# Performance work log

Measured on AMD Instinct MI355X. Metric: run time of the kernel, lower is better.

The kernel has to match this reference:

```python
import jax, jax.numpy as jnp
import numpy as np
import math

B, S, D, H = 2, 2048, 1024, 16
DH = D // H
MASK_VALUE = -1e6


def setup_inputs() -> dict:
    key = jax.random.key(0)
    ks = jax.random.split(key, 6)
    x = jax.random.normal(ks[0], (B, S, D), dtype=jnp.float32)
    scale = 1.0 / math.sqrt(D)
    Wq = jax.random.normal(ks[1], (D, D), dtype=jnp.float32) * scale
    Wk = jax.random.normal(ks[2], (D, D), dtype=jnp.float32) * scale
    Wv = jax.random.normal(ks[3], (D, D), dtype=jnp.float32) * scale
    Wo = jax.random.normal(ks[4], (D, D), dtype=jnp.float32) * scale
    valid_lens = jax.random.randint(ks[5], (B,), 1, S + 1, dtype=jnp.int32)
    return {"x": x, "Wq": Wq, "Wk": Wk, "Wv": Wv, "Wo": Wo, "valid_lens": valid_lens}


def reference(x, Wq, Wk, Wv, Wo, valid_lens):
    # Projections (Linear with bias=False): [B,S,D] -> split into H heads of DH
    def split_heads(y):
        return y.reshape(B, S, H, DH).transpose(0, 2, 1, 3)  # [B,H,S,DH]

    q = split_heads(x @ Wq)
    k = split_heads(x @ Wk)
    v = split_heads(x @ Wv)

    # scores [B,H,Sq,Sk]; masking depends only on key position per batch
    scores = jnp.einsum("bhqd,bhkd->bhqk", q, k) / math.sqrt(DH)
    key_pos = jnp.arange(S, dtype=jnp.int32)  # [Sk]
    mask = key_pos[None, None, None, :] < valid_lens[:, None, None, None]
    scores = jnp.where(mask, scores, MASK_VALUE)
    attn = jax.nn.softmax(scores, axis=-1)  # dropout is identity in eval

    out = jnp.einsum("bhqk,bhkd->bhqd", attn, v)  # [B,H,S,DH]
    out = out.transpose(0, 2, 1, 3).reshape(B, S, D)  # concat heads
    return out @ Wo
```

## Files before the change

### kernel.cpp

```cpp
#include <hip/hip_runtime.h>

#define Bdim 2
#define Sdim 2048
#define Ddim 1024
#define Hdim 16

typedef unsigned short u16;
typedef u16 u16x8 __attribute__((ext_vector_type(8)));
typedef u16 u16x4 __attribute__((ext_vector_type(4)));
typedef unsigned u32x4 __attribute__((ext_vector_type(4)));
typedef __bf16 bf16x8 __attribute__((ext_vector_type(8)));
typedef float f32x4 __attribute__((ext_vector_type(4)));
typedef float f32x16 __attribute__((ext_vector_type(16)));

static __device__ __forceinline__ u16 f2bf(float f) {
  unsigned u = __float_as_uint(f);
  u += 0x7fffu + ((u >> 16) & 1u);
  return (u16)(u >> 16);
}
static __device__ __forceinline__ float bf2f(u16 v) {
  return __uint_as_float((unsigned)v << 16);
}
static __device__ __forceinline__ bf16x8 asbf(u16x8 v) {
  return __builtin_bit_cast(bf16x8, v);
}
static __device__ __forceinline__ f32x4 mfma16(bf16x8 a, bf16x8 b, f32x4 c) {
  return __builtin_amdgcn_mfma_f32_16x16x32_bf16(a, b, c, 0, 0, 0);
}
static __device__ __forceinline__ f32x16 mfma32(bf16x8 a, bf16x8 b, f32x16 c) {
  return __builtin_amdgcn_mfma_f32_32x32x16_bf16(a, b, c, 0, 0, 0);
}

__global__ __launch_bounds__(256) void cvtx(const float* __restrict__ x,
                                            u16* __restrict__ xb) {
  int i = blockIdx.x * 256 + threadIdx.x;
  const float4* xp = (const float4*)x;
  float4 a = xp[2 * i], b = xp[2 * i + 1];
  u16x8 o;
  o[0] = f2bf(a.x); o[1] = f2bf(a.y); o[2] = f2bf(a.z); o[3] = f2bf(a.w);
  o[4] = f2bf(b.x); o[5] = f2bf(b.y); o[6] = f2bf(b.z); o[7] = f2bf(b.w);
  ((u16x8*)xb)[i] = o;
}

__global__ __launch_bounds__(256) void transw(
    const float* __restrict__ W0, const float* __restrict__ W1,
    const float* __restrict__ W2, const float* __restrict__ W3,
    u16* __restrict__ T0, u16* __restrict__ T1,
    u16* __restrict__ T2, u16* __restrict__ T3) {
  const float* W = blockIdx.z == 0 ? W0 : blockIdx.z == 1 ? W1 : blockIdx.z == 2 ? W2 : W3;
  u16* T = blockIdx.z == 0 ? T0 : blockIdx.z == 1 ? T1 : blockIdx.z == 2 ? T2 : T3;
  __shared__ float tile[32][33];
  const int t = threadIdx.x;
  const int k0 = blockIdx.x * 32, n0 = blockIdx.y * 32;
  const int r = t >> 3, cq = (t & 7) * 4;
  float4 v = *(const float4*)(W + (size_t)(k0 + r) * Ddim + n0 + cq);
  tile[r][cq] = v.x; tile[r][cq + 1] = v.y; tile[r][cq + 2] = v.z; tile[r][cq + 3] = v.w;
  __syncthreads();
  u16x4 ov;
  ov[0] = f2bf(tile[cq][r]);
  ov[1] = f2bf(tile[cq + 1][r]);
  ov[2] = f2bf(tile[cq + 2][r]);
  ov[3] = f2bf(tile[cq + 3][r]);
  *(u16x4*)(T + (size_t)(n0 + r) * Ddim + k0 + cq) = ov;
}

__global__ __launch_bounds__(256) void vtrans(const u16* __restrict__ V,
                                              u16* __restrict__ Vt) {
  __shared__ u16 tile[32][72];
  const int t = threadIdx.x;
  const int s0 = blockIdx.x * 32;
  const int bh = blockIdx.y, b = bh >> 4, h = bh & 15;
  {
    int sl = t >> 3, dq = (t & 7) * 8;
    u16x8 v = *(const u16x8*)(V + (size_t)(b * Sdim + s0 + sl) * Ddim + h * 64 + dq);
    *(u16x8*)(&tile[sl][dq]) = v;
  }
  __syncthreads();
  {
    int dl = t >> 2, sq = (t & 3) * 8;
    u16x8 v;
#pragma unroll
    for (int i = 0; i < 8; i++) v[i] = tile[sq + i][dl];
    int s = s0 + sq;
    int kt = s >> 6, c = (s >> 3) & 7;
    *(u16x8*)(Vt + ((((size_t)bh * 32 + kt) * 8 + c) * 64 + dl) * 8) = v;
  }
}

__global__ __launch_bounds__(256) void tilek(const u16* __restrict__ K,
                                             u16* __restrict__ Kt) {
  int tid = blockIdx.x * 256 + threadIdx.x;
  int row = tid & 63;
  int c = (tid >> 6) & 7;
  int kt = (tid >> 9) & 31;
  int bh = tid >> 14;
  int b = bh >> 4, h = bh & 15;
  u16x8 kc = *(const u16x8*)(K + (size_t)(b * Sdim + kt * 64 + row) * Ddim + h * 64 + c * 8);
  ((u16x8*)Kt)[tid] = kc;
}

template <bool F32OUT>
__global__ __launch_bounds__(256) void gemm128(
    const u16* __restrict__ A,
    const u16* __restrict__ Bt0, const u16* __restrict__ Bt1, const u16* __restrict__ Bt2,
    void* __restrict__ C0v, void* __restrict__ C1v, void* __restrict__ C2v) {
  __shared__ u16 As[128 * 64];
  __shared__ u16 Bs[128 * 64];
  const int zz = blockIdx.y >> 3;
  const u16* Bt = (zz == 0) ? Bt0 : (zz == 1) ? Bt1 : Bt2;
  void* Cv = (zz == 0) ? C0v : (zz == 1) ? C1v : C2v;

  const int t = threadIdx.x;
  const int lane = t & 63, w = t >> 6;
  const int wm = w >> 1, wn = w & 1;
  const int c = lane & 15, g = lane >> 4;
  const int m0 = blockIdx.x * 128, n0 = (blockIdx.y & 7) * 128;
  const float oscale = (!F32OUT && zz == 0) ? 0.125f : 1.0f;

  const f32x4 zv = {0.f, 0.f, 0.f, 0.f};
  f32x4 acc[4][4];
#pragma unroll
  for (int m = 0; m < 4; m++)
#pragma unroll
    for (int n = 0; n < 4; n++) acc[m][n] = zv;

  for (int kt = 0; kt < 1024; kt += 64) {
    __syncthreads();
#pragma unroll
    for (int i = 0; i < 4; i++) {
      int idx = t + 256 * i;
      int row = idx >> 3, ch = idx & 7;
      int sw = (ch ^ (row & 7)) * 8;
      u16x8 va = *(const u16x8*)(A + (size_t)(m0 + row) * 1024 + kt + ch * 8);
      *(u16x8*)(As + row * 64 + sw) = va;
      u16x8 vb = *(const u16x8*)(Bt + (size_t)(n0 + row) * 1024 + kt + ch * 8);
      *(u16x8*)(Bs + row * 64 + sw) = vb;
    }
    __syncthreads();
#pragma unroll
    for (int kh = 0; kh < 2; kh++) {
      bf16x8 af[4], bfr[4];
#pragma unroll
      for (int m = 0; m < 4; m++) {
        int row = wm * 64 + m * 16 + c;
        int chr = kh * 4 + g;
        af[m] = asbf(*(const u16x8*)(As + row * 64 + ((chr ^ (row & 7)) * 8)));
      }
#pragma unroll
      for (int n = 0; n < 4; n++) {
        int row = wn * 64 + n * 16 + c;
        int chr = kh * 4 + g;
        bfr[n] = asbf(*(const u16x8*)(Bs + row * 64 + ((chr ^ (row & 7)) * 8)));
      }
#pragma unroll
      for (int m = 0; m < 4; m++)
#pragma unroll
        for (int n = 0; n < 4; n++) acc[m][n] = mfma16(af[m], bfr[n], acc[m][n]);
    }
  }
#pragma unroll
  for (int m = 0; m < 4; m++)
#pragma unroll
    for (int n = 0; n < 4; n++)
#pragma unroll
      for (int r = 0; r < 4; r++) {
        int row = m0 + wm * 64 + m * 16 + 4 * g + r;
        int col = n0 + wn * 64 + n * 16 + c;
        if (F32OUT)
          ((float*)Cv)[(size_t)row * 1024 + col] = acc[m][n][r];
        else
          ((u16*)Cv)[(size_t)row * 1024 + col] = f2bf(acc[m][n][r] * oscale);
      }
}

__global__ __launch_bounds__(64, 4) void attn_kernel(
    const u16* __restrict__ Q, const u16* __restrict__ Kt,
    const u16* __restrict__ Vt, const int* __restrict__ vlen,
    u16* __restrict__ O, u16* __restrict__ Opart, float2* __restrict__ mlp) {
  __shared__ u16 ot[32][72];
  const int lane = threadIdx.x;
  const int q = lane & 31, hi = lane >> 5;
  const int bh = blockIdx.y, b = bh >> 4, h = bh & 15;
  const int q0 = blockIdx.x * 32;
  const int nv = vlen[b];
  const int NS = gridDim.z, z = blockIdx.z;

  bf16x8 qf[4];
  {
    const u16* qp = Q + (size_t)(b * Sdim + q0 + q) * Ddim + h * 64 + hi * 8;
#pragma unroll
    for (int s = 0; s < 4; s++) qf[s] = asbf(*(const u16x8*)(qp + s * 16));
  }

  f32x16 o0, o1;
#pragma unroll
  for (int r = 0; r < 16; r++) { o0[r] = 0.f; o1[r] = 0.f; }
  float m = -3.0e38f, l = 0.f;

  const int nt = (nv + 63) >> 6;
  const int chunk = (nt + NS - 1) / NS;
  const int t0 = z * chunk;
  const int t1 = min(nt, t0 + chunk);
  for (int kt = t0; kt < t1; ++kt) {
    const int k0 = kt * 64;
    const u16* Ktile = Kt + ((size_t)bh * 32 + kt) * 4096;
    const u16* Vtile = Vt + ((size_t)bh * 32 + kt) * 4096;
    f32x16 sc[2];
#pragma unroll
    for (int kb = 0; kb < 2; kb++) {
      f32x16 acc;
#pragma unroll
      for (int r = 0; r < 16; r++) acc[r] = 0.f;
#pragma unroll
      for (int s = 0; s < 4; s++) {
        bf16x8 kf = asbf(*(const u16x8*)(Ktile + (2 * s + hi) * 512 + (kb * 32 + q) * 8));
        acc = mfma32(kf, qf[s], acc);
      }
      sc[kb] = acc;
    }
    if (k0 + 64 > nv) {
#pragma unroll
      for (int kb = 0; kb < 2; kb++)
#pragma unroll
        for (int r = 0; r < 16; r++) {
          int key = k0 + kb * 32 + (r & 3) + 8 * (r >> 2) + 4 * hi;
          if (key >= nv) sc[kb][r] = -1e30f;
        }
    }
    float mx[16];
#pragma unroll
    for (int r = 0; r < 16; r++) mx[r] = fmaxf(sc[0][r], sc[1][r]);
#pragma unroll
    for (int st = 8; st > 0; st >>= 1)
#pragma unroll
      for (int r = 0; r < st; r++) mx[r] = fmaxf(mx[r], mx[r + st]);
    float tm = fmaxf(mx[0], __shfl_xor(mx[0], 32));
    if (!__all(tm <= m + 8.f)) {
      float mn = fmaxf(m, tm);
      float al = __expf(m - mn);
#pragma unroll
      for (int r = 0; r < 16; r++) { o0[r] *= al; o1[r] *= al; }
      l *= al;
      m = mn;
    }
    unsigned pw[4][4];
    float s0 = 0.f, s1 = 0.f, s2 = 0.f, s3 = 0.f;
#pragma unroll
    for (int kb = 0; kb < 2; kb++)
#pragma unroll
      for (int hh = 0; hh < 2; hh++)
#pragma unroll
        for (int wi = 0; wi < 4; wi++) {
          float e0 = __expf(sc[kb][hh * 8 + wi * 2] - m);
          float e1 = __expf(sc[kb][hh * 8 + wi * 2 + 1] - m);
          if (wi == 0) s0 += e0 + e1;
          else if (wi == 1) s1 += e0 + e1;
          else if (wi == 2) s2 += e0 + e1;
          else s3 += e0 + e1;
          asm("v_cvt_pk_bf16_f32 %0, %1, %2"
              : "=v"(pw[kb * 2 + hh][wi]) : "v"(e0), "v"(e1));
        }
    float ssum = (s0 + s1) + (s2 + s3);
    ssum += __shfl_xor(ssum, 32);
    l += ssum;
#pragma unroll
    for (int f = 0; f < 4; f++) {
      asm("v_permlane32_swap_b32 %0, %1" : "+v"(pw[f][0]), "+v"(pw[f][2]));
      asm("v_permlane32_swap_b32 %0, %1" : "+v"(pw[f][1]), "+v"(pw[f][3]));
    }
#pragma unroll
    for (int f = 0; f < 4; f++) {
      u32x4 wv = {pw[f][0], pw[f][1], pw[f][2], pw[f][3]};
      bf16x8 pa = __builtin_bit_cast(bf16x8, wv);
      bf16x8 va = asbf(*(const u16x8*)(Vtile + (2 * f + hi) * 512 + q * 8));
      bf16x8 vb = asbf(*(const u16x8*)(Vtile + (2 * f + hi) * 512 + (32 + q) * 8));
      o0 = mfma32(va, pa, o0);
      o1 = mfma32(vb, pa, o1);
    }
  }
  const float scale = (NS == 1) ? (1.f / l) : 1.f;
#pragma unroll
  for (int r = 0; r < 16; r++) {
    const int dh = (r & 3) + 8 * (r >> 2) + 4 * hi;
    ot[q][dh] = f2bf(o0[r] * scale);
    ot[q][32 + dh] = f2bf(o1[r] * scale);
  }
  asm volatile("s_waitcnt lgkmcnt(0)" ::: "memory");
  __builtin_amdgcn_sched_barrier(0);
  if (NS == 1) {
    u16* op = O + (size_t)(b * Sdim + q0 + q) * Ddim + h * 64 + hi * 32;
#pragma unroll
    for (int j = 0; j < 4; j++)
      *(u16x8*)(op + j * 8) = *(const u16x8*)(&ot[q][hi * 32 + j * 8]);
  } else {
    u16* op = Opart + ((size_t)(z * 32 + bh) * Sdim + q0 + q) * 64 + hi * 32;
#pragma unroll
    for (int j = 0; j < 4; j++)
      *(u16x8*)(op + j * 8) = *(const u16x8*)(&ot[q][hi * 32 + j * 8]);
    if (hi == 0)
      mlp[(size_t)(z * 32 + bh) * Sdim + q0 + q] = make_float2(m, l);
  }
}

template <int NS>
__global__ __launch_bounds__(256) void attn_combine(
    const u16* __restrict__ Opart, const float2* __restrict__ mlp,
    u16* __restrict__ O) {
  const int t = threadIdx.x;
  const int bh = blockIdx.y, b = bh >> 4, h = bh & 15;
  const int q = blockIdx.x * 32 + (t >> 3);
  const int d0 = (t & 7) * 8;
  float2 ml[NS];
  float M = -3.0e38f;
#pragma unroll
  for (int z = 0; z < NS; z++) {
    ml[z] = mlp[(size_t)(z * 32 + bh) * Sdim + q];
    M = fmaxf(M, ml[z].x);
  }
  float acc[8];
#pragma unroll
  for (int i = 0; i < 8; i++) acc[i] = 0.f;
  float wsum = 0.f;
#pragma unroll
  for (int z = 0; z < NS; z++) {
    float w = __expf(ml[z].x - M);
    wsum += w * ml[z].y;
    u16x8 ov = *(const u16x8*)(Opart + ((size_t)(z * 32 + bh) * Sdim + q) * 64 + d0);
#pragma unroll
    for (int i = 0; i < 8; i++) acc[i] += w * bf2f(ov[i]);
  }
  const float inv = 1.f / wsum;
  u16x8 res;
#pragma unroll
  for (int i = 0; i < 8; i++) res[i] = f2bf(acc[i] * inv);
  *(u16x8*)(O + ((size_t)b * Sdim + q) * Ddim + h * 64 + d0) = res;
}

extern "C" void kernel_launch(void* const* d_in, const int* in_sizes, int n_in,
                              void* d_out, int out_size, void* d_ws, size_t ws_size,
                              hipStream_t stream) {
  const float* x = (const float*)d_in[0];
  const float* Wq = (const float*)d_in[1];
  const float* Wk = (const float*)d_in[2];
  const float* Wv = (const float*)d_in[3];
  const float* Wo = (const float*)d_in[4];
  const int* vl = (const int*)d_in[5];
  float* out = (float*)d_out;

  char* ws = (char*)d_ws;
  const size_t SZ_X = (size_t)Bdim * Sdim * Ddim * sizeof(u16);
  const size_t SZ_W = (size_t)Ddim * Ddim * sizeof(u16);
  u16* xb = (u16*)ws; ws += SZ_X;
  u16* WqT = (u16*)ws; ws += SZ_W;
  u16* WkT = (u16*)ws; ws += SZ_W;
  u16* WvT = (u16*)ws; ws += SZ_W;
  u16* WoT = (u16*)ws; ws += SZ_W;
  u16* Qb = (u16*)ws; ws += SZ_X;
  u16* Kb = (u16*)ws; ws += SZ_X;
  u16* Vb = (u16*)ws; ws += SZ_X;
  u16* Ob = (u16*)ws; ws += SZ_X;
  u16* Ktb = (u16*)ws; ws += SZ_X;
  u16* Vtb = (u16*)ws; ws += SZ_X;

  const size_t PER_SPLIT = (size_t)Bdim * Hdim * Sdim * 64 * sizeof(u16) +
                           (size_t)Bdim * Hdim * Sdim * sizeof(float2);
  size_t used = (size_t)(ws - (char*)d_ws);
  size_t avail = (ws_size > used) ? ws_size - used : 0;
  int NS = (avail >= 4 * PER_SPLIT) ? 4 : (avail >= 2 * PER_SPLIT) ? 2 : 1;
  u16* Opart = (u16*)ws;
  float2* mlp = (float2*)(ws + (size_t)NS * Bdim * Hdim * Sdim * 64 * sizeof(u16));

  cvtx<<<dim3((Bdim * Sdim * Ddim) / (8 * 256)), 256, 0, stream>>>(x, xb);
  transw<<<dim3(32, 32, 4), 256, 0, stream>>>(Wq, Wk, Wv, Wo, WqT, WkT, WvT, WoT);
  gemm128<false><<<dim3(32, 24), 256, 0, stream>>>(xb, WqT, WkT, WvT, Qb, Kb, Vb);
  vtrans<<<dim3(Sdim / 32, Bdim * Hdim), 256, 0, stream>>>(Vb, Vtb);
  tilek<<<dim3((Bdim * Sdim * Ddim / 8) / 256), 256, 0, stream>>>(Kb, Ktb);
  attn_kernel<<<dim3(Sdim / 32, Bdim * Hdim, NS), 64, 0, stream>>>(Qb, Ktb, Vtb, vl, Ob,
                                                                   Opart, mlp);
  if (NS == 4)
    attn_combine<4><<<dim3(Sdim / 32, Bdim * Hdim), 256, 0, stream>>>(Opart, mlp, Ob);
  else if (NS == 2)
    attn_combine<2><<<dim3(Sdim / 32, Bdim * Hdim), 256, 0, stream>>>(Opart, mlp, Ob);
  gemm128<true><<<dim3(32, 8), 256, 0, stream>>>(Ob, WoT, WoT, WoT, out, out, out);
}
```

Baseline: 130.3 us.

## Store GEMM operands in MFMA-fragment order and load fragments directly from global

```diff
diff --git a/kernel.cpp b/kernel.cpp
--- a/kernel.cpp
+++ b/kernel.cpp
@@ -31,15 +31,22 @@
   return __builtin_amdgcn_mfma_f32_32x32x16_bf16(a, b, c, 0, 0, 0);
 }
 
+static __device__ __forceinline__ size_t ftcell(int R, int k) {
+  return ((((((size_t)(R >> 7) * 16 + (k >> 6)) * 2 + ((R >> 6) & 1)) * 4 +
+            ((R >> 4) & 3)) * 2 + ((k >> 5) & 1)) * 4 + ((k >> 3) & 3)) * 16 +
+         (R & 15);
+}
+
 __global__ __launch_bounds__(256) void cvtx(const float* __restrict__ x,
-                                            u16* __restrict__ xb) {
+                                            u16* __restrict__ xf) {
   int i = blockIdx.x * 256 + threadIdx.x;
   const float4* xp = (const float4*)x;
   float4 a = xp[2 * i], b = xp[2 * i + 1];
   u16x8 o;
   o[0] = f2bf(a.x); o[1] = f2bf(a.y); o[2] = f2bf(a.z); o[3] = f2bf(a.w);
   o[4] = f2bf(b.x); o[5] = f2bf(b.y); o[6] = f2bf(b.z); o[7] = f2bf(b.w);
-  ((u16x8*)xb)[i] = o;
+  int R = i >> 7, k = (i & 127) * 8;
+  ((u16x8*)xf)[ftcell(R, k)] = o;
 }
 
 __global__ __launch_bounds__(256) void transw(
@@ -61,7 +68,8 @@
   ov[1] = f2bf(tile[cq + 1][r]);
   ov[2] = f2bf(tile[cq + 2][r]);
   ov[3] = f2bf(tile[cq + 3][r]);
-  *(u16x4*)(T + (size_t)(n0 + r) * Ddim + k0 + cq) = ov;
+  int n = n0 + r, k = k0 + cq;
+  *(u16x4*)(T + ftcell(n, k) * 8 + (k & 7)) = ov;
 }
 
 __global__ __launch_bounds__(256) void vtrans(const u16* __restrict__ V,
@@ -100,12 +108,10 @@
 }
 
 template <bool F32OUT>
-__global__ __launch_bounds__(256) void gemm128(
+__global__ __launch_bounds__(256, 4) void gemm128(
     const u16* __restrict__ A,
     const u16* __restrict__ Bt0, const u16* __restrict__ Bt1, const u16* __restrict__ Bt2,
     void* __restrict__ C0v, void* __restrict__ C1v, void* __restrict__ C2v) {
-  __shared__ u16 As[128 * 64];
-  __shared__ u16 Bs[128 * 64];
   const int zz = blockIdx.y >> 3;
   const u16* Bt = (zz == 0) ? Bt0 : (zz == 1) ? Bt1 : Bt2;
   void* Cv = (zz == 0) ? C0v : (zz == 1) ? C1v : C2v;
@@ -114,7 +120,7 @@
   const int lane = t & 63, w = t >> 6;
   const int wm = w >> 1, wn = w & 1;
   const int c = lane & 15, g = lane >> 4;
-  const int m0 = blockIdx.x * 128, n0 = (blockIdx.y & 7) * 128;
+  const int mb = blockIdx.x, nb = blockIdx.y & 7;
   const float oscale = (!F32OUT && zz == 0) ? 0.125f : 1.0f;
 
   const f32x4 zv = {0.f, 0.f, 0.f, 0.f};
@@ -124,33 +130,21 @@
 #pragma unroll
     for (int n = 0; n < 4; n++) acc[m][n] = zv;
 
-  for (int kt = 0; kt < 1024; kt += 64) {
-    __syncthreads();
-#pragma unroll
-    for (int i = 0; i < 4; i++) {
-      int idx = t + 256 * i;
-      int row = idx >> 3, ch = idx & 7;
-      int sw = (ch ^ (row & 7)) * 8;
-      u16x8 va = *(const u16x8*)(A + (size_t)(m0 + row) * 1024 + kt + ch * 8);
-      *(u16x8*)(As + row * 64 + sw) = va;
-      u16x8 vb = *(const u16x8*)(Bt + (size_t)(n0 + row) * 1024 + kt + ch * 8);
-      *(u16x8*)(Bs + row * 64 + sw) = vb;
-    }
-    __syncthreads();
+  const u16* Abase = A + (size_t)lane * 8;
+  const u16* Bbase = Bt + (size_t)lane * 8;
+  for (int kt = 0; kt < 16; ++kt) {
 #pragma unroll
     for (int kh = 0; kh < 2; kh++) {
       bf16x8 af[4], bfr[4];
 #pragma unroll
       for (int m = 0; m < 4; m++) {
-        int row = wm * 64 + m * 16 + c;
-        int chr = kh * 4 + g;
-        af[m] = asbf(*(const u16x8*)(As + row * 64 + ((chr ^ (row & 7)) * 8)));
+        size_t X = ((((size_t)mb * 16 + kt) * 2 + wm) * 4 + m) * 2 + kh;
+        af[m] = asbf(*(const u16x8*)(Abase + X * 512));
       }
 #pragma unroll
       for (int n = 0; n < 4; n++) {
-        int row = wn * 64 + n * 16 + c;
-        int chr = kh * 4 + g;
-        bfr[n] = asbf(*(const u16x8*)(Bs + row * 64 + ((chr ^ (row & 7)) * 8)));
+        size_t Y = ((((size_t)nb * 16 + kt) * 2 + wn) * 4 + n) * 2 + kh;
+        bfr[n] = asbf(*(const u16x8*)(Bbase + Y * 512));
       }
 #pragma unroll
       for (int m = 0; m < 4; m++)
@@ -164,8 +158,8 @@
     for (int n = 0; n < 4; n++)
 #pragma unroll
       for (int r = 0; r < 4; r++) {
-        int row = m0 + wm * 64 + m * 16 + 4 * g + r;
-        int col = n0 + wn * 64 + n * 16 + c;
+        int row = mb * 128 + wm * 64 + m * 16 + 4 * g + r;
+        int col = nb * 128 + wn * 64 + n * 16 + c;
         if (F32OUT)
           ((float*)Cv)[(size_t)row * 1024 + col] = acc[m][n][r];
         else
@@ -288,10 +282,12 @@
   asm volatile("s_waitcnt lgkmcnt(0)" ::: "memory");
   __builtin_amdgcn_sched_barrier(0);
   if (NS == 1) {
-    u16* op = O + (size_t)(b * Sdim + q0 + q) * Ddim + h * 64 + hi * 32;
-#pragma unroll
-    for (int j = 0; j < 4; j++)
-      *(u16x8*)(op + j * 8) = *(const u16x8*)(&ot[q][hi * 32 + j * 8]);
+    int R = b * Sdim + q0 + q;
+#pragma unroll
+    for (int j = 0; j < 4; j++) {
+      int k = h * 64 + hi * 32 + j * 8;
+      ((u16x8*)O)[ftcell(R, k)] = *(const u16x8*)(&ot[q][hi * 32 + j * 8]);
+    }
   } else {
     u16* op = Opart + ((size_t)(z * 32 + bh) * Sdim + q0 + q) * 64 + hi * 32;
 #pragma unroll
@@ -333,7 +329,8 @@
   u16x8 res;
 #pragma unroll
   for (int i = 0; i < 8; i++) res[i] = f2bf(acc[i] * inv);
-  *(u16x8*)(O + ((size_t)b * Sdim + q) * Ddim + h * 64 + d0) = res;
+  int R = b * Sdim + q, k = h * 64 + d0;
+  ((u16x8*)O)[ftcell(R, k)] = res;
 }
 
 extern "C" void kernel_launch(void* const* d_in, const int* in_sizes, int n_in,
@@ -350,7 +347,7 @@
   char* ws = (char*)d_ws;
   const size_t SZ_X = (size_t)Bdim * Sdim * Ddim * sizeof(u16);
   const size_t SZ_W = (size_t)Ddim * Ddim * sizeof(u16);
-  u16* xb = (u16*)ws; ws += SZ_X;
+  u16* xf = (u16*)ws; ws += SZ_X;
   u16* WqT = (u16*)ws; ws += SZ_W;
   u16* WkT = (u16*)ws; ws += SZ_W;
   u16* WvT = (u16*)ws; ws += SZ_W;
@@ -358,7 +355,7 @@
   u16* Qb = (u16*)ws; ws += SZ_X;
   u16* Kb = (u16*)ws; ws += SZ_X;
   u16* Vb = (u16*)ws; ws += SZ_X;
-  u16* Ob = (u16*)ws; ws += SZ_X;
+  u16* Obf = (u16*)ws; ws += SZ_X;
   u16* Ktb = (u16*)ws; ws += SZ_X;
   u16* Vtb = (u16*)ws; ws += SZ_X;
 
@@ -370,16 +367,16 @@
   u16* Opart = (u16*)ws;
   float2* mlp = (float2*)(ws + (size_t)NS * Bdim * Hdim * Sdim * 64 * sizeof(u16));
 
-  cvtx<<<dim3((Bdim * Sdim * Ddim) / (8 * 256)), 256, 0, stream>>>(x, xb);
+  cvtx<<<dim3((Bdim * Sdim * Ddim) / (8 * 256)), 256, 0, stream>>>(x, xf);
   transw<<<dim3(32, 32, 4), 256, 0, stream>>>(Wq, Wk, Wv, Wo, WqT, WkT, WvT, WoT);
-  gemm128<false><<<dim3(32, 24), 256, 0, stream>>>(xb, WqT, WkT, WvT, Qb, Kb, Vb);
+  gemm128<false><<<dim3(32, 24), 256, 0, stream>>>(xf, WqT, WkT, WvT, Qb, Kb, Vb);
   vtrans<<<dim3(Sdim / 32, Bdim * Hdim), 256, 0, stream>>>(Vb, Vtb);
   tilek<<<dim3((Bdim * Sdim * Ddim / 8) / 256), 256, 0, stream>>>(Kb, Ktb);
-  attn_kernel<<<dim3(Sdim / 32, Bdim * Hdim, NS), 64, 0, stream>>>(Qb, Ktb, Vtb, vl, Ob,
+  attn_kernel<<<dim3(Sdim / 32, Bdim * Hdim, NS), 64, 0, stream>>>(Qb, Ktb, Vtb, vl, Obf,
                                                                    Opart, mlp);
   if (NS == 4)
-    attn_combine<4><<<dim3(Sdim / 32, Bdim * Hdim), 256, 0, stream>>>(Opart, mlp, Ob);
+    attn_combine<4><<<dim3(Sdim / 32, Bdim * Hdim), 256, 0, stream>>>(Opart, mlp, Obf);
   else if (NS == 2)
-    attn_combine<2><<<dim3(Sdim / 32, Bdim * Hdim), 256, 0, stream>>>(Opart, mlp, Ob);
-  gemm128<true><<<dim3(32, 8), 256, 0, stream>>>(Ob, WoT, WoT, WoT, out, out, out);
-}
+    attn_combine<2><<<dim3(Sdim / 32, Bdim * Hdim), 256, 0, stream>>>(Opart, mlp, Obf);
+  gemm128<true><<<dim3(32, 8), 256, 0, stream>>>(Obf, WoT, WoT, WoT, out, out, out);
+}
```

Result: slower. 160.9 us (+23.4%).
